# Kernel tuning notes

Hardware: AMD Instinct MI355X
Metric: run time of the kernel (lower is better)

Reference implementation:

```python
import jax, jax.numpy as jnp
import numpy as np

BETA = 0.95      # config.snn_beta
THR = 1.0        # snntorch Leaky default threshold
SLOPE = 10.0     # config.surrogate_slope (fast_sigmoid)
T = 16           # config.snn_timesteps
A_PLUS, A_MINUS = 0.008, 0.01
ELIG_DECAY = 0.95

# Heaviside spike with fast-sigmoid surrogate gradient: d/dm = 1/(slope*|m-thr|+1)^2
@jax.custom_vjp
def spike_fn(m):
    return (m > THR).astype(m.dtype)

def _spk_fwd(m):
    return spike_fn(m), m

def _spk_bwd(m, g):
    return (g / (SLOPE * jnp.abs(m - THR) + 1.0) ** 2,)

spike_fn.defvjp(_spk_fwd, _spk_bwd)


def setup_inputs() -> dict:
    key = jax.random.key(0)
    ks = jax.random.split(key, 7)
    B, S, H, A = 65536, 25, 64, 4

    def lin_w(k, o, i):
        lim = 1.0 / np.sqrt(i)
        return jax.random.uniform(k, (o, i), jnp.float32, -lim, lim)

    def lin_b(k, o, i):
        lim = 1.0 / np.sqrt(i)
        return jax.random.uniform(k, (o,), jnp.float32, -lim, lim)

    return {
        "x": jax.random.normal(ks[0], (B, S), jnp.float32),
        "W1": lin_w(ks[1], H, S), "b1": lin_b(ks[2], H, S),
        "W2": lin_w(ks[3], H, H), "b2": lin_b(ks[4], H, H),
        "W3": lin_w(ks[5], A, H), "b3": lin_b(ks[6], A, H),
        "elig0": jnp.zeros((A, H), jnp.float32),  # eligibility trace (fc3.out, fc3.in)
    }


def reference(x, W1, b1, W2, b2, W3, b3, elig0):
    B = x.shape[0]
    H = W1.shape[0]
    A = W3.shape[0]
    cur1 = x @ W1.T + b1  # input current is identical every timestep

    def step(carry, _):
        m1, m2, m3, elig, acc = carry
        m1 = BETA * m1 + cur1
        s1 = spike_fn(m1)
        m1 = m1 - s1 * THR
        m2 = BETA * m2 + s1 @ W2.T + b2
        s2 = spike_fn(m2)
        m2 = m2 - s2 * THR
        m3 = BETA * m3 + s2 @ W3.T + b3
        s3 = spike_fn(m3)
        m3 = m3 - s3 * THR
        pre = jax.lax.stop_gradient(s2).mean(0)   # [H]
        post = jax.lax.stop_gradient(s3).mean(0)  # [A]
        elig = ELIG_DECAY * elig + (A_PLUS - A_MINUS) * jnp.outer(post, pre)
        return (m1, m2, m3, elig, acc + s3), None

    init = (
        jnp.zeros((B, H), x.dtype),
        jnp.zeros((B, H), x.dtype),
        jnp.zeros((B, A), x.dtype),
        elig0,
        jnp.zeros((B, A), x.dtype),
    )
    (_, _, _, elig, acc), _ = jax.lax.scan(step, init, None, length=T)
    readout = acc / T  # mean over timesteps of spk3
    probs = jax.nn.softmax(readout, axis=-1)
    return probs, elig
```

## Files before the change

kernel.cpp:

```cpp
#include <hip/hip_runtime.h>

#define T_STEPS 16
#define H 64
#define S_IN 25
#define A_OUT 4
#define NB 65536
#define UPW 8
#define WPB 8
#define EPB 128

typedef unsigned long long ull;

__device__ __forceinline__ float fmaf_(float a, float b, float c) { return __builtin_fmaf(a, b, c); }

__global__ void snn_prep(const float* __restrict__ W2, const float* __restrict__ W3,
                         float* __restrict__ W2T, float* __restrict__ W3T) {
    int i = blockIdx.x * blockDim.x + threadIdx.x;
    if (i < H * H) { int h = i >> 6, k = i & 63; W2T[k * H + h] = W2[h * H + k]; }
    if (i < A_OUT * H) { int a = i >> 6, h = i & 63; W3T[h * A_OUT + a] = W3[a * H + h]; }
}

__global__ __launch_bounds__(512, 4) void snn_main(
    const float* __restrict__ x,
    const float* __restrict__ W1, const float* __restrict__ b1,
    const float* __restrict__ W2T, const float* __restrict__ b2,
    const float* __restrict__ W3T, const float* __restrict__ b3,
    float* __restrict__ out, int* __restrict__ g_pre, int* __restrict__ g_post)
{
#pragma clang fp contract(off)
    __shared__ float4 w3s[H];
    __shared__ unsigned int s1buf[2][WPB][EPB];
    __shared__ unsigned int s2buf[2][WPB][EPB];
    __shared__ float m3acc[EPB][8];
    __shared__ int lds_pre[T_STEPS * H];
    __shared__ int lds_post[T_STEPS * A_OUT];

    const int tid = threadIdx.x;
    if (tid < H) w3s[tid] = reinterpret_cast<const float4*>(W3T)[tid];
    for (int i = tid; i < T_STEPS * H; i += 512) lds_pre[i] = 0;
    if (tid < T_STEPS * A_OUT) lds_post[tid] = 0;
    for (int i = tid; i < EPB * 8; i += 512) (&m3acc[0][0])[i] = 0.0f;

    const int lane  = tid & 63;
    const int wq    = __builtin_amdgcn_readfirstlane(tid >> 6);
    const int hbase = UPW * wq;
    const int bA    = blockIdx.x * EPB + lane;
    const int bB    = bA + 64;

    float cur1A[UPW], cur1B[UPW];
    {
        float xv[S_IN];
        #pragma unroll
        for (int s = 0; s < S_IN; ++s) xv[s] = x[bA * S_IN + s];
        #pragma unroll
        for (int j = 0; j < UPW; ++j) {
            int h = hbase + j;
            float acc = 0.0f;
            #pragma unroll
            for (int s = 0; s < S_IN; ++s) acc = fmaf_(xv[s], W1[h * S_IN + s], acc);
            cur1A[j] = acc + b1[h];
        }
        #pragma unroll
        for (int s = 0; s < S_IN; ++s) xv[s] = x[bB * S_IN + s];
        #pragma unroll
        for (int j = 0; j < UPW; ++j) {
            int h = hbase + j;
            float acc = 0.0f;
            #pragma unroll
            for (int s = 0; s < S_IN; ++s) acc = fmaf_(xv[s], W1[h * S_IN + s], acc);
            cur1B[j] = acc + b1[h];
        }
    }

    float m1A[UPW], m1B[UPW], m2A[UPW], m2B[UPW];
    #pragma unroll
    for (int j = 0; j < UPW; ++j) { m1A[j] = 0.0f; m1B[j] = 0.0f; m2A[j] = 0.0f; m2B[j] = 0.0f; }

    __syncthreads();

    {
        unsigned int sA = 0u, sB = 0u;
        #pragma unroll
        for (int j = 0; j < UPW; ++j) {
            float ma = 0.95f * m1A[j]; ma = ma + cur1A[j];
            bool pa = ma > 1.0f; m1A[j] = pa ? (ma - 1.0f) : ma; sA |= (pa ? 1u : 0u) << j;
            float mb = 0.95f * m1B[j]; mb = mb + cur1B[j];
            bool pb = mb > 1.0f; m1B[j] = pb ? (mb - 1.0f) : mb; sB |= (pb ? 1u : 0u) << j;
        }
        s1buf[0][wq][lane] = sA;
        s1buf[0][wq][lane + 64] = sB;
    }
    __syncthreads();

    for (int t = 0; t < T_STEPS; ++t) {
        const int slot = t & 1;

        unsigned int mloA, mhiA, mloB, mhiB;
        {
            unsigned int a0 = s1buf[slot][0][lane], a1 = s1buf[slot][1][lane];
            unsigned int a2 = s1buf[slot][2][lane], a3 = s1buf[slot][3][lane];
            unsigned int a4 = s1buf[slot][4][lane], a5 = s1buf[slot][5][lane];
            unsigned int a6 = s1buf[slot][6][lane], a7 = s1buf[slot][7][lane];
            mloA = a0 | (a1 << 8) | (a2 << 16) | (a3 << 24);
            mhiA = a4 | (a5 << 8) | (a6 << 16) | (a7 << 24);
            unsigned int c0 = s1buf[slot][0][lane + 64], c1 = s1buf[slot][1][lane + 64];
            unsigned int c2 = s1buf[slot][2][lane + 64], c3 = s1buf[slot][3][lane + 64];
            unsigned int c4 = s1buf[slot][4][lane + 64], c5 = s1buf[slot][5][lane + 64];
            unsigned int c6 = s1buf[slot][6][lane + 64], c7 = s1buf[slot][7][lane + 64];
            mloB = c0 | (c1 << 8) | (c2 << 16) | (c3 << 24);
            mhiB = c4 | (c5 << 8) | (c6 << 16) | (c7 << 24);
        }

        #pragma unroll
        for (int j = 0; j < UPW; ++j) { m2A[j] = 0.95f * m2A[j]; m2B[j] = 0.95f * m2B[j]; }

        #pragma unroll 8
        for (int k = 0; k < 32; ++k) {
            const float sfA = (float)((mloA >> k) & 1u);
            const float sfB = (float)((mloB >> k) & 1u);
            const float* wr = W2T + k * H + hbase;
            #pragma unroll
            for (int j = 0; j < UPW; ++j) {
                const float w = wr[j];
                m2A[j] = fmaf_(sfA, w, m2A[j]);
                m2B[j] = fmaf_(sfB, w, m2B[j]);
            }
        }
        #pragma unroll 8
        for (int k = 0; k < 32; ++k) {
            const float sfA = (float)((mhiA >> k) & 1u);
            const float sfB = (float)((mhiB >> k) & 1u);
            const float* wr = W2T + (k + 32) * H + hbase;
            #pragma unroll
            for (int j = 0; j < UPW; ++j) {
                const float w = wr[j];
                m2A[j] = fmaf_(sfA, w, m2A[j]);
                m2B[j] = fmaf_(sfB, w, m2B[j]);
            }
        }

        unsigned int s2A = 0u, s2B = 0u;
        int myCnt = 0;
        #pragma unroll
        for (int j = 0; j < UPW; ++j) {
            float ma = m2A[j] + b2[hbase + j];
            bool pa = ma > 1.0f;
            m2A[j] = ma - (pa ? 1.0f : 0.0f);
            s2A |= (pa ? 1u : 0u) << j;
            float mb = m2B[j] + b2[hbase + j];
            bool pb = mb > 1.0f;
            m2B[j] = mb - (pb ? 1.0f : 0.0f);
            s2B |= (pb ? 1u : 0u) << j;
            int cnt = (int)__popcll(__ballot(pa)) + (int)__popcll(__ballot(pb));
            myCnt = (lane == j) ? cnt : myCnt;
        }
        s2buf[slot][wq][lane] = s2A;
        s2buf[slot][wq][lane + 64] = s2B;
        if (lane < UPW) lds_pre[t * H + hbase + lane] = myCnt;

        if (t < T_STEPS - 1) {
            unsigned int sA = 0u, sB = 0u;
            #pragma unroll
            for (int j = 0; j < UPW; ++j) {
                float ma = 0.95f * m1A[j]; ma = ma + cur1A[j];
                bool pa = ma > 1.0f; m1A[j] = pa ? (ma - 1.0f) : ma; sA |= (pa ? 1u : 0u) << j;
                float mb = 0.95f * m1B[j]; mb = mb + cur1B[j];
                bool pb = mb > 1.0f; m1B[j] = pb ? (mb - 1.0f) : mb; sB |= (pb ? 1u : 0u) << j;
            }
            s1buf[slot ^ 1][wq][lane] = sA;
            s1buf[slot ^ 1][wq][lane + 64] = sB;
        }
        __syncthreads();

        const int duty = wq & 3;
        if (duty == (t & 3)) {
            const int el = (wq < 4) ? lane : (lane + 64);
            unsigned int q0 = s2buf[slot][0][el], q1 = s2buf[slot][1][el];
            unsigned int q2 = s2buf[slot][2][el], q3 = s2buf[slot][3][el];
            unsigned int q4 = s2buf[slot][4][el], q5 = s2buf[slot][5][el];
            unsigned int q6 = s2buf[slot][6][el], q7 = s2buf[slot][7][el];
            ull s2v = (ull)(q0 | (q1 << 8) | (q2 << 16) | (q3 << 24))
                    | ((ull)(q4 | (q5 << 8) | (q6 << 16) | (q7 << 24)) << 32);
            float m3[A_OUT], ac[A_OUT];
            #pragma unroll
            for (int a = 0; a < A_OUT; ++a) { m3[a] = 0.95f * m3acc[el][a]; ac[a] = m3acc[el][4 + a]; }
            for (int h = 0; h < H; ++h) {
                float s2f = (float)((unsigned)s2v & 1u);
                s2v >>= 1;
                const float4 w = w3s[h];
                m3[0] = fmaf_(s2f, w.x, m3[0]);
                m3[1] = fmaf_(s2f, w.y, m3[1]);
                m3[2] = fmaf_(s2f, w.z, m3[2]);
                m3[3] = fmaf_(s2f, w.w, m3[3]);
            }
            int myPost = 0;
            #pragma unroll
            for (int a = 0; a < A_OUT; ++a) {
                float m = m3[a] + b3[a];
                bool sp = m > 1.0f;
                float s3f = sp ? 1.0f : 0.0f;
                m3[a] = m - s3f;
                ac[a] = ac[a] + s3f;
                int c = (int)__popcll(__ballot(sp));
                myPost = (lane == a) ? c : myPost;
            }
            if (lane < A_OUT) atomicAdd(&lds_post[t * A_OUT + lane], myPost);
            if (t == T_STEPS - 1) {
                float r0 = ac[0] * 0.0625f, r1 = ac[1] * 0.0625f;
                float r2 = ac[2] * 0.0625f, r3 = ac[3] * 0.0625f;
                float mx = fmaxf(fmaxf(r0, r1), fmaxf(r2, r3));
                float e0 = expf(r0 - mx), e1 = expf(r1 - mx);
                float e2 = expf(r2 - mx), e3 = expf(r3 - mx);
                float s = ((e0 + e1) + e2) + e3;
                reinterpret_cast<float4*>(out)[blockIdx.x * EPB + el] =
                    make_float4(e0 / s, e1 / s, e2 / s, e3 / s);
            } else {
                #pragma unroll
                for (int a = 0; a < A_OUT; ++a) { m3acc[el][a] = m3[a]; m3acc[el][4 + a] = ac[a]; }
            }
        }
    }

    __syncthreads();
    for (int i = tid; i < T_STEPS * H; i += 512) atomicAdd(&g_pre[i], lds_pre[i]);
    if (tid < T_STEPS * A_OUT) atomicAdd(&g_post[tid], lds_post[tid]);
}

__global__ void snn_elig(const int* __restrict__ g_pre, const int* __restrict__ g_post,
                         const float* __restrict__ elig0, float* __restrict__ out) {
#pragma clang fp contract(off)
    int i = threadIdx.x;
    int a = i >> 6, h = i & 63;
    float e = elig0[i];
    const float invB = 1.0f / 65536.0f;
    for (int t = 0; t < T_STEPS; ++t) {
        float pre  = (float)g_pre[t * H + h] * invB;
        float post = (float)g_post[t * A_OUT + a] * invB;
        e = 0.95f * e + (-0.002f) * (post * pre);
    }
    out[NB * A_OUT + i] = e;
}

extern "C" void kernel_launch(void* const* d_in, const int* in_sizes, int n_in,
                              void* d_out, int out_size, void* d_ws, size_t ws_size,
                              hipStream_t stream) {
    const float* x     = (const float*)d_in[0];
    const float* W1    = (const float*)d_in[1];
    const float* b1    = (const float*)d_in[2];
    const float* W2    = (const float*)d_in[3];
    const float* b2    = (const float*)d_in[4];
    const float* W3    = (const float*)d_in[5];
    const float* b3    = (const float*)d_in[6];
    const float* elig0 = (const float*)d_in[7];
    float* out = (float*)d_out;

    char* ws = (char*)d_ws;
    int*   g_pre  = (int*)(ws);
    int*   g_post = (int*)(ws + 4096);
    float* W2T    = (float*)(ws + 8192);
    float* W3T    = (float*)(ws + 8192 + 16384);

    (void)hipMemsetAsync(ws, 0, 4096 + 256, stream);
    snn_prep<<<17, 256, 0, stream>>>(W2, W3, W2T, W3T);
    snn_main<<<NB / EPB, 512, 0, stream>>>(x, W1, b1, W2T, b2, W3T, b3, out, g_pre, g_post);
    snn_elig<<<1, 256, 0, stream>>>(g_pre, g_post, elig0, out);
}
```

Baseline: 171.5 us.

## Precompute all layer-1 spike bits up front into packed LDS bytes

Layer 1 depends only on the constant input current, so all timesteps of its spikes are now computed before the main loop and stored as bytes in a [T][EPB][8] LDS array. Each timestep then reads one 64-bit word per element instead of eight 32-bit words plus shift-or assembly. This frees the m1/cur1 registers during the main loop and removes layer-1 work from the synchronized per-step critical path. In exchange it adds 16KB of LDS and risks bank conflicts on the byte stores, which may reduce occupancy at 4 blocks per CU.

Result: faster. 166.7 us (-2.8%).

```diff
diff --git a/kernel.cpp b/kernel.cpp
--- a/kernel.cpp
+++ b/kernel.cpp
@@ -28,8 +28,8 @@
     float* __restrict__ out, int* __restrict__ g_pre, int* __restrict__ g_post)
 {
 #pragma clang fp contract(off)
+    __shared__ unsigned char s1bits[T_STEPS][EPB][8];
     __shared__ float4 w3s[H];
-    __shared__ unsigned int s1buf[2][WPB][EPB];
     __shared__ unsigned int s2buf[2][WPB][EPB];
     __shared__ float m3acc[EPB][8];
     __shared__ int lds_pre[T_STEPS * H];
@@ -47,8 +47,8 @@
     const int bA    = blockIdx.x * EPB + lane;
     const int bB    = bA + 64;
 
-    float cur1A[UPW], cur1B[UPW];
     {
+        float cur1A[UPW], cur1B[UPW];
         float xv[S_IN];
         #pragma unroll
         for (int s = 0; s < S_IN; ++s) xv[s] = x[bA * S_IN + s];
@@ -70,46 +70,37 @@
             for (int s = 0; s < S_IN; ++s) acc = fmaf_(xv[s], W1[h * S_IN + s], acc);
             cur1B[j] = acc + b1[h];
         }
+
+        float m1A[UPW], m1B[UPW];
+        #pragma unroll
+        for (int j = 0; j < UPW; ++j) { m1A[j] = 0.0f; m1B[j] = 0.0f; }
+        for (int t = 0; t < T_STEPS; ++t) {
+            unsigned int sA = 0u, sB = 0u;
+            #pragma unroll
+            for (int j = 0; j < UPW; ++j) {
+                float ma = 0.95f * m1A[j]; ma = ma + cur1A[j];
+                bool pa = ma > 1.0f; m1A[j] = pa ? (ma - 1.0f) : ma; sA |= (pa ? 1u : 0u) << j;
+                float mb = 0.95f * m1B[j]; mb = mb + cur1B[j];
+                bool pb = mb > 1.0f; m1B[j] = pb ? (mb - 1.0f) : mb; sB |= (pb ? 1u : 0u) << j;
+            }
+            s1bits[t][lane][wq]      = (unsigned char)sA;
+            s1bits[t][lane + 64][wq] = (unsigned char)sB;
+        }
     }
 
-    float m1A[UPW], m1B[UPW], m2A[UPW], m2B[UPW];
+    float m2A[UPW], m2B[UPW];
     #pragma unroll
-    for (int j = 0; j < UPW; ++j) { m1A[j] = 0.0f; m1B[j] = 0.0f; m2A[j] = 0.0f; m2B[j] = 0.0f; }
-
-    __syncthreads();
-
-    {
-        unsigned int sA = 0u, sB = 0u;
-        #pragma unroll
-        for (int j = 0; j < UPW; ++j) {
-            float ma = 0.95f * m1A[j]; ma = ma + cur1A[j];
-            bool pa = ma > 1.0f; m1A[j] = pa ? (ma - 1.0f) : ma; sA |= (pa ? 1u : 0u) << j;
-            float mb = 0.95f * m1B[j]; mb = mb + cur1B[j];
-            bool pb = mb > 1.0f; m1B[j] = pb ? (mb - 1.0f) : mb; sB |= (pb ? 1u : 0u) << j;
-        }
-        s1buf[0][wq][lane] = sA;
-        s1buf[0][wq][lane + 64] = sB;
-    }
+    for (int j = 0; j < UPW; ++j) { m2A[j] = 0.0f; m2B[j] = 0.0f; }
+
     __syncthreads();
 
     for (int t = 0; t < T_STEPS; ++t) {
         const int slot = t & 1;
 
-        unsigned int mloA, mhiA, mloB, mhiB;
-        {
-            unsigned int a0 = s1buf[slot][0][lane], a1 = s1buf[slot][1][lane];
-            unsigned int a2 = s1buf[slot][2][lane], a3 = s1buf[slot][3][lane];
-            unsigned int a4 = s1buf[slot][4][lane], a5 = s1buf[slot][5][lane];
-            unsigned int a6 = s1buf[slot][6][lane], a7 = s1buf[slot][7][lane];
-            mloA = a0 | (a1 << 8) | (a2 << 16) | (a3 << 24);
-            mhiA = a4 | (a5 << 8) | (a6 << 16) | (a7 << 24);
-            unsigned int c0 = s1buf[slot][0][lane + 64], c1 = s1buf[slot][1][lane + 64];
-            unsigned int c2 = s1buf[slot][2][lane + 64], c3 = s1buf[slot][3][lane + 64];
-            unsigned int c4 = s1buf[slot][4][lane + 64], c5 = s1buf[slot][5][lane + 64];
-            unsigned int c6 = s1buf[slot][6][lane + 64], c7 = s1buf[slot][7][lane + 64];
-            mloB = c0 | (c1 << 8) | (c2 << 16) | (c3 << 24);
-            mhiB = c4 | (c5 << 8) | (c6 << 16) | (c7 << 24);
-        }
+        const ull mA = *reinterpret_cast<const ull*>(&s1bits[t][lane][0]);
+        const ull mB = *reinterpret_cast<const ull*>(&s1bits[t][lane + 64][0]);
+        const unsigned int mloA = (unsigned int)mA, mhiA = (unsigned int)(mA >> 32);
+        const unsigned int mloB = (unsigned int)mB, mhiB = (unsigned int)(mB >> 32);
 
         #pragma unroll
         for (int j = 0; j < UPW; ++j) { m2A[j] = 0.95f * m2A[j]; m2B[j] = 0.95f * m2B[j]; }
@@ -158,18 +149,6 @@
         s2buf[slot][wq][lane + 64] = s2B;
         if (lane < UPW) lds_pre[t * H + hbase + lane] = myCnt;
 
-        if (t < T_STEPS - 1) {
-            unsigned int sA = 0u, sB = 0u;
-            #pragma unroll
-            for (int j = 0; j < UPW; ++j) {
-                float ma = 0.95f * m1A[j]; ma = ma + cur1A[j];
-                bool pa = ma > 1.0f; m1A[j] = pa ? (ma - 1.0f) : ma; sA |= (pa ? 1u : 0u) << j;
-                float mb = 0.95f * m1B[j]; mb = mb + cur1B[j];
-                bool pb = mb > 1.0f; m1B[j] = pb ? (mb - 1.0f) : mb; sB |= (pb ? 1u : 0u) << j;
-            }
-            s1buf[slot ^ 1][wq][lane] = sA;
-            s1buf[slot ^ 1][wq][lane + 64] = sB;
-        }
         __syncthreads();
 
         const int duty = wq & 3;
```
